# Optimization experiments

Hardware: AMD Instinct MI355X
Metric: run time of the kernel (lower is better)

Reference implementation:

```python
import jax, jax.numpy as jnp
import numpy as np

N = 50000      # nodes (atoms)
E = 800000     # edges (avg degree 16)
Z = 10         # num_elements
C = 32         # hidden channels (scalar multiplicity of hidden_irreps)
NB = 8         # num_bessel
H = 64         # radial MLP hidden
CORR = 3       # correlation order of product basis
MLPH = 16      # MLP_irreps = 16x0e
R_MAX = 5.0
AVG_NN = 16.0
P_CUT = 5      # num_polynomial_cutoff
N_SH = 9       # spherical harmonics up to l=2
L_OF_LM = jnp.array([0, 1, 1, 1, 2, 2, 2, 2, 2])  # l index of each lm component


def _sph_harm(u):
    # real spherical harmonics, e3nn 'component' normalization, up to l=2. u: [E,3] unit vectors
    x, y, z = u[:, 0], u[:, 1], u[:, 2]
    s3, s5, s15 = 3.0 ** 0.5, 5.0 ** 0.5, 15.0 ** 0.5
    return jnp.stack([
        jnp.ones_like(x),
        s3 * x, s3 * y, s3 * z,
        s15 * x * y, s15 * y * z, 0.5 * s5 * (3.0 * z * z - 1.0),
        s15 * x * z, 0.5 * s15 * (x * x - y * y),
    ], axis=-1)


def _poly_cutoff(r):
    # polynomial envelope, p=5, zero beyond r_max
    p = float(P_CUT)
    u = r / R_MAX
    f = (1.0 - 0.5 * (p + 1.0) * (p + 2.0) * u ** P_CUT
         + p * (p + 2.0) * u ** (P_CUT + 1)
         - 0.5 * p * (p + 1.0) * u ** (P_CUT + 2))
    return f * (u < 1.0)


def setup_inputs() -> dict:
    key = jax.random.key(0)
    ks = jax.random.split(key, 24)
    elems = jax.random.randint(ks[0], (N,), 0, Z)
    node_attrs = jax.nn.one_hot(elems, Z, dtype=jnp.float32)
    positions = jax.random.uniform(ks[1], (N, 3), dtype=jnp.float32, minval=0.0, maxval=10.0)
    senders = jax.random.randint(ks[2], (E,), 0, N)
    receivers = jax.random.randint(ks[3], (E,), 0, N)

    def rn(k, shape, fan_in):
        return jax.random.normal(k, shape, dtype=jnp.float32) / np.sqrt(fan_in)

    params = {
        'W_embed': rn(ks[4], (Z, C), Z),
        'atomic_E': jax.random.normal(ks[5], (Z,), dtype=jnp.float32),
        'Wr0': rn(ks[6], (2, NB, H), NB),
        'Wr1': rn(ks[7], (2, H, H), H),
        'Wr2': rn(ks[8], (2, H, H), H),
        'Wr3': rn(ks[9], (2, H, 3 * C), H),
        'Wlin': rn(ks[10], (2, C, C), C),
        'Wsc': rn(ks[11], (2, Z, C, C), C),
        'Wprod': rn(ks[12], (2, 3, C, C), C),
        'Wp': rn(ks[13], (2, CORR, Z, C), Z),
        'w_ro1': rn(ks[14], (C,), C),
        'W_m1': rn(ks[15], (C, MLPH), C),
        'w_m2': rn(ks[16], (MLPH,), MLPH),
    }
    return {'node_attrs': node_attrs, 'positions': positions,
            'senders': senders, 'receivers': receivers, **params}


def reference(node_attrs, positions, W_embed, atomic_E, Wr0, Wr1, Wr2, Wr3,
              Wlin, Wsc, Wprod, Wp, w_ro1, W_m1, w_m2, senders, receivers):
    silu = jax.nn.silu
    # --- edge geometry ---
    vec = positions[receivers] - positions[senders]          # [E,3]
    r = jnp.sqrt(jnp.sum(vec * vec, axis=-1) + 1e-12)        # [E]
    unit = vec / r[:, None]
    sh = _sph_harm(unit)                                     # [E, 9]
    fcut = _poly_cutoff(r)                                   # [E]

    # --- radial embedding: Bessel basis * polynomial cutoff ---
    n = jnp.arange(1, NB + 1, dtype=jnp.float32)
    bessel = jnp.sqrt(2.0 / R_MAX) * jnp.sin(n[None, :] * jnp.pi * r[:, None] / R_MAX) / r[:, None]
    R = bessel * fcut[:, None]                               # [E, NB]

    # --- ZBL pair repulsion ---
    z_arr = jnp.arange(1, Z + 1, dtype=jnp.float32)
    zq = node_attrs @ z_arr                                  # [N]
    zi, zj = zq[senders], zq[receivers]
    a = 0.46850 / (zi ** 0.23 + zj ** 0.23)
    xx = r / a
    phi = (0.1818 * jnp.exp(-3.2 * xx) + 0.5099 * jnp.exp(-0.9423 * xx)
           + 0.2802 * jnp.exp(-0.4029 * xx) + 0.02817 * jnp.exp(-0.2016 * xx))
    v_zbl = 14.3996 * zi * zj / r * phi * fcut
    pair_energy = 0.5 * jax.ops.segment_sum(v_zbl, receivers, num_segments=N)  # [N]

    # --- atomic reference energies + node embedding ---
    node_energy = node_attrs @ atomic_E + pair_energy        # [N]
    h = node_attrs @ W_embed                                 # [N, C] scalar node feats

    feats_list = []
    for i in range(2):
        # radial MLP -> per-edge, per-l, per-channel tensor-product weights
        w = silu(R @ Wr0[i])
        w = silu(w @ Wr1[i])
        w = silu(w @ Wr2[i])
        w = (w @ Wr3[i]).reshape(E, 3, C)                    # [E, l, C]
        w_lm = w[:, L_OF_LM, :]                              # [E, 9, C]
        # message: channel-mixed sender scalars x spherical harmonics x radial weights
        h1 = h @ Wlin[i]                                     # [N, C]
        msg = sh[:, :, None] * h1[senders][:, None, :] * w_lm  # [E, 9, C]
        A = jax.ops.segment_sum(msg, receivers, num_segments=N) / AVG_NN  # [N, 9, C]
        # element-conditioned residual (self-connection)
        sc = jnp.einsum('nz,nc,zcd->nd', node_attrs, h, Wsc[i])  # [N, C]
        # equivariant product basis: per-l linear + symmetric contraction on scalars
        Wlm = Wprod[i][L_OF_LM]                              # [9, C, C]
        out = jnp.einsum('nmc,mcd->nmd', A, Wlm)             # [N, 9, C]
        A0 = A[:, 0, :]
        poly = jnp.zeros_like(A0)
        for k in range(CORR):
            poly = poly + jnp.einsum('nz,zc->nc', node_attrs, Wp[i, k]) * A0 ** (k + 1)
        h_scalar = out[:, 0, :] + poly + sc                  # [N, C]
        # readout
        if i == 0:
            e = h_scalar @ w_ro1
        else:
            e = silu(h_scalar @ W_m1) @ w_m2
        node_energy = node_energy + e
        h = h_scalar
        feats_list.append(out.at[:, 0, :].set(h_scalar).reshape(N, N_SH * C))

    node_feats = jnp.concatenate(feats_list, axis=-1)        # [N, 2*9*C]
    return node_energy, node_feats
```

## Files before the change

### kernel.cpp

```cpp
#include <hip/hip_runtime.h>
#include <math.h>

static constexpr int Cdim = 32;
static constexpr int NBES = 8;
static constexpr int HDIM = 64;
static constexpr int ZDIM = 10;
static constexpr int TBLN = 8192;

typedef _Float16 half8 __attribute__((ext_vector_type(8)));
typedef _Float16 half4 __attribute__((ext_vector_type(4)));
typedef float floatx4 __attribute__((ext_vector_type(4)));

__device__ __forceinline__ float silu_f(float x) {
    return x / (1.0f + __expf(-x));
}

__device__ __forceinline__ float4 shfl4(float4 v, int src) {
    return make_float4(__shfl(v.x, src), __shfl(v.y, src),
                       __shfl(v.z, src), __shfl(v.w, src));
}

__global__ __launch_bounds__(320)
void k_wemb(const float* __restrict__ W_embed, const float* __restrict__ Wlin0,
            float* __restrict__ EW)
{
    int t = threadIdx.x;
    if (t >= ZDIM * Cdim) return;
    int z = t >> 5, d = t & 31;
    float acc = 0.f;
    #pragma unroll
    for (int c = 0; c < Cdim; ++c) acc += W_embed[z * Cdim + c] * Wlin0[c * Cdim + d];
    EW[t] = acc;
}

__global__ __launch_bounds__(256)
void k_node_init(const float* __restrict__ attrs, const float* __restrict__ pos,
                 const float* __restrict__ W_embed, const float* __restrict__ atomE,
                 const float* __restrict__ EW, int* __restrict__ elem,
                 float* __restrict__ energy, int* __restrict__ deg,
                 float4* __restrict__ pos4, _Float16* __restrict__ h16cur,
                 _Float16* __restrict__ h1a16, int N)
{
    int n = blockIdx.x * blockDim.x + threadIdx.x;
    if (n >= N) return;
    int e = 0; float best = -1.0f;
    #pragma unroll
    for (int z = 0; z < ZDIM; ++z) {
        float v = attrs[n * ZDIM + z];
        if (v > best) { best = v; e = z; }
    }
    elem[n] = e;
    #pragma unroll
    for (int c = 0; c < Cdim; c += 4) {
        half4 ph, p1;
        #pragma unroll
        for (int q = 0; q < 4; ++q) {
            ph[q] = (_Float16)W_embed[e * Cdim + c + q];
            p1[q] = (_Float16)EW[e * Cdim + c + q];
        }
        *(half4*)(h16cur + (size_t)n * Cdim + c) = ph;
        *(half4*)(h1a16  + (size_t)n * Cdim + c) = p1;
    }
    energy[n] = atomE[e];
    deg[n] = 0;
    float zf = (float)(e + 1);
    pos4[n] = make_float4(pos[3*n+0], pos[3*n+1], pos[3*n+2],
                          4.0f * zf + powf(zf, 0.23f));
}

__global__ __launch_bounds__(256)
void k_filter(const float4* __restrict__ pos4, const int* __restrict__ snd,
              const int* __restrict__ rcv, unsigned long long* __restrict__ mask,
              int* __restrict__ deg, float4* __restrict__ quadE,
              float* __restrict__ zslotE, int E)
{
    int e = blockIdx.x * blockDim.x + threadIdx.x;
    int ec = min(e, E - 1);
    int s = snd[ec], t = rcv[ec];
    float4 pt = pos4[t], ps = pos4[s];
    float dx = pt.x - ps.x, dy = pt.y - ps.y, dz = pt.z - ps.z;
    float d2 = dx*dx + dy*dy + dz*dz;
    bool pred = (e < E) && (d2 < 25.0f);
    unsigned long long m = __ballot(pred ? 1 : 0);
    if ((threadIdx.x & 63) == 0) mask[e >> 6] = m;
    if (pred) {
        atomicAdd(&deg[t], 1);
        float r  = sqrtf(d2 + 1e-12f);
        float inv_r = 1.0f / r;
        quadE[e] = make_float4(dx * inv_r, dy * inv_r, dz * inv_r, r);
        float tz = floorf(pt.w * 0.25f), tz23 = pt.w - 4.0f * tz;
        float sz = floorf(ps.w * 0.25f), sz23 = ps.w - 4.0f * sz;
        float u  = r * 0.2f;
        float u2 = u*u, u5 = u2*u2*u;
        float fcut = 1.0f - 21.0f*u5 + 35.0f*u5*u - 15.0f*u5*u2;
        float xx = r * (sz23 + tz23) * 2.134471718f;
        float phi = 0.1818f*__expf(-3.2f*xx) + 0.5099f*__expf(-0.9423f*xx)
                  + 0.2802f*__expf(-0.4029f*xx) + 0.02817f*__expf(-0.2016f*xx);
        zslotE[e] = tz * sz * inv_r * phi * fcut;
    }
}

__global__ __launch_bounds__(1024)
void k_scan1(const int* __restrict__ deg, int* __restrict__ rowptr,
             int* __restrict__ bsum, int* __restrict__ bhist,
             int* __restrict__ myslot, int N)
{
    __shared__ int wsum[16];
    __shared__ int lhist[64];
    int tid = threadIdx.x, lane = tid & 63, w = tid >> 6;
    if (tid < 64) lhist[tid] = 0;
    __syncthreads();
    int i = blockIdx.x * 1024 + tid;
    int v = (i < N) ? deg[i] : 0;
    if (i < N) myslot[i] = atomicAdd(&lhist[min(v, 63)], 1);
    int s = v;
    #pragma unroll
    for (int d = 1; d < 64; d <<= 1) {
        int u = __shfl_up(s, d);
        if (lane >= d) s += u;
    }
    if (lane == 63) wsum[w] = s;
    __syncthreads();
    if (w == 0 && lane < 16) {
        int x = wsum[lane];
        #pragma unroll
        for (int d = 1; d < 16; d <<= 1) {
            int u = __shfl_up(x, d);
            if (lane >= d) x += u;
        }
        wsum[lane] = x;
    }
    __syncthreads();
    int wave_off = (w == 0) ? 0 : wsum[w - 1];
    if (i < N) rowptr[i] = wave_off + (s - v);
    if (tid == 0) bsum[blockIdx.x] = wsum[15];
    if (tid < 64) bhist[blockIdx.x * 64 + tid] = lhist[tid];
}

__global__ __launch_bounds__(128)
void k_scan2(int* __restrict__ bsum, int nb, int* __restrict__ bhist,
             int* __restrict__ rowptrN)
{
    int tid = threadIdx.x;
    int lane = tid & 63;
    if (tid < 64) {
        int v = (lane < nb) ? bsum[lane] : 0;
        int s = v;
        #pragma unroll
        for (int d = 1; d < 64; d <<= 1) {
            int u = __shfl_up(s, d);
            if (lane >= d) s += u;
        }
        if (lane < nb) bsum[lane] = s - v;
        if (lane == 63) *rowptrN = s;
    } else {
        int b = lane;
        int run = 0;
        for (int blk = 0; blk < nb; ++blk) {
            int t = bhist[blk * 64 + b];
            bhist[blk * 64 + b] = run;
            run += t;
        }
        int s = run;
        #pragma unroll
        for (int d = 1; d < 64; d <<= 1) {
            int u = __shfl_up(s, d);
            if (lane >= d) s += u;
        }
        int excl = s - run;
        for (int blk = 0; blk < nb; ++blk) bhist[blk * 64 + b] += excl;
    }
}

__global__ __launch_bounds__(1024)
void k_scan3(const int* __restrict__ deg, int* __restrict__ rowptr,
             int* __restrict__ cursor, const int* __restrict__ bsum,
             const int* __restrict__ bhist, const int* __restrict__ myslot,
             int* __restrict__ perm, int N)
{
    int i = blockIdx.x * 1024 + threadIdx.x;
    if (i >= N) return;
    int rv = rowptr[i] + bsum[blockIdx.x];
    rowptr[i] = rv;
    cursor[i] = rv;
    int b = min(deg[i], 63);
    perm[bhist[blockIdx.x * 64 + b] + myslot[i]] = i;
}

__global__ __launch_bounds__(256)
void k_place(const int* __restrict__ snd, const int* __restrict__ rcv,
             const unsigned long long* __restrict__ mask,
             const float4* __restrict__ quadE, const float* __restrict__ zslotE,
             int* __restrict__ cursor, int* __restrict__ eS,
             float4* __restrict__ quad, float* __restrict__ zslot, int E)
{
    int e = blockIdx.x * blockDim.x + threadIdx.x;
    if (e >= E) return;
    if (!((mask[e >> 6] >> (e & 63)) & 1ull)) return;
    int t = rcv[e];
    int slot = atomicAdd(&cursor[t], 1);
    eS[slot] = snd[e];
    quad[slot] = quadE[e];
    zslot[slot] = zslotE[e];
}

__global__ __launch_bounds__(256, 2)
void k_table(const float* __restrict__ W0, const float* __restrict__ W1,
             const float* __restrict__ W2, const float* __restrict__ W3,
             _Float16* __restrict__ table)
{
    __shared__ __align__(16) _Float16 sWt0[64*32];
    __shared__ __align__(16) _Float16 sWt1[64*64];
    __shared__ __align__(16) _Float16 sWt2[64*64];
    __shared__ __align__(16) _Float16 sWt3[96*64];
    __shared__ __align__(16) _Float16 sAct[4][64*64];

    for (int idx = threadIdx.x; idx < 64*32; idx += 256) {
        int n = idx >> 5, k = idx & 31;
        float v = (k < NBES) ? W0[k*64 + n] : 0.f;
        *(_Float16*)((char*)sWt0 + n*64 + ((k*2) ^ ((n&3)<<4))) = (_Float16)v;
    }
    for (int idx = threadIdx.x; idx < 64*64; idx += 256) {
        int k = idx >> 6, n = idx & 63;
        int byo = n*128 + ((k*2) ^ ((n&7)<<4));
        *(_Float16*)((char*)sWt1 + byo) = (_Float16)W1[idx];
        *(_Float16*)((char*)sWt2 + byo) = (_Float16)W2[idx];
    }
    for (int idx = threadIdx.x; idx < 64*96; idx += 256) {
        int k = idx / 96, n = idx - k*96;
        *(_Float16*)((char*)sWt3 + n*128 + ((k*2) ^ ((n&7)<<4))) = (_Float16)W3[idx];
    }
    __syncthreads();

    const int wid = threadIdx.x >> 6, lane = threadIdx.x & 63;
    const int l15 = lane & 15, lh = lane >> 4;
    char* actc = (char*)sAct[wid];

    half8 w1f[4], w2f[4][2], w3f[4][2], w4f[6][2];
    #pragma unroll
    for (int nt = 0; nt < 4; ++nt) {
        int nn = nt*16 + l15;
        w1f[nt] = *(half8*)((char*)sWt0 + nn*64 + ((lh*16) ^ ((nn&3)<<4)));
        #pragma unroll
        for (int ks = 0; ks < 2; ++ks) {
            w2f[nt][ks] = *(half8*)((char*)sWt1 + nn*128 + ((ks*64 + lh*16) ^ ((nn&7)<<4)));
            w3f[nt][ks] = *(half8*)((char*)sWt2 + nn*128 + ((ks*64 + lh*16) ^ ((nn&7)<<4)));
        }
    }
    #pragma unroll
    for (int nt = 0; nt < 6; ++nt) {
        int nn = nt*16 + l15;
        #pragma unroll
        for (int ks = 0; ks < 2; ++ks)
            w4f[nt][ks] = *(half8*)((char*)sWt3 + nn*128 + ((ks*64 + lh*16) ^ ((nn&7)<<4)));
    }

    int c0 = (blockIdx.x*4 + wid)*64;
    {
        int q = c0 + lane;
        float r = (q + 0.5f) * (5.0f / (float)TBLN);
        float inv_r = 1.0f / r;
        float u  = r * 0.2f;
        float u2 = u*u, u5 = u2*u2*u;
        float fcut = 1.0f - 21.0f*u5 + 35.0f*u5*u - 15.0f*u5*u2;
        float coef = 0.632455532f * inv_r * fcut;
        half8 rv;
        #pragma unroll
        for (int j = 0; j < NBES; ++j)
            rv[j] = (_Float16)(coef * __sinf((float)(j+1) * 0.628318531f * r));
        {
            int sw = (lane & 7) << 4;
            half8 zz = {};
            *(half8*)(actc + lane*128 + ( 0 ^ sw)) = rv;
            *(half8*)(actc + lane*128 + (16 ^ sw)) = zz;
            *(half8*)(actc + lane*128 + (32 ^ sw)) = zz;
            *(half8*)(actc + lane*128 + (48 ^ sw)) = zz;
        }
        __builtin_amdgcn_sched_barrier(0);

        #pragma unroll
        for (int mt = 0; mt < 4; ++mt) {
            int rr = mt*16 + l15;
            int swz = (rr & 7) << 4;
            half8 act = *(half8*)(actc + rr*128 + ((lh*16) ^ swz));
            #pragma unroll
            for (int nt = 0; nt < 4; ++nt) {
                floatx4 z = {0.f,0.f,0.f,0.f};
                floatx4 d = __builtin_amdgcn_mfma_f32_16x16x32_f16(w1f[nt], act, z, 0,0,0);
                half4 pk;
                #pragma unroll
                for (int j = 0; j < 4; ++j) pk[j] = (_Float16)silu_f(d[j]);
                *(half4*)(actc + rr*128 + ((nt*32 + lh*8) ^ swz)) = pk;
            }
        }
        __builtin_amdgcn_sched_barrier(0);

        #pragma unroll
        for (int layer = 0; layer < 2; ++layer) {
            #pragma unroll
            for (int mt = 0; mt < 4; ++mt) {
                int rr = mt*16 + l15;
                int swz = (rr & 7) << 4;
                half8 a0 = *(half8*)(actc + rr*128 + ((      lh*16) ^ swz));
                half8 a1 = *(half8*)(actc + rr*128 + ((64 + lh*16) ^ swz));
                #pragma unroll
                for (int nt = 0; nt < 4; ++nt) {
                    floatx4 z = {0.f,0.f,0.f,0.f};
                    if (layer == 0) {
                        z = __builtin_amdgcn_mfma_f32_16x16x32_f16(w2f[nt][0], a0, z, 0,0,0);
                        z = __builtin_amdgcn_mfma_f32_16x16x32_f16(w2f[nt][1], a1, z, 0,0,0);
                    } else {
                        z = __builtin_amdgcn_mfma_f32_16x16x32_f16(w3f[nt][0], a0, z, 0,0,0);
                        z = __builtin_amdgcn_mfma_f32_16x16x32_f16(w3f[nt][1], a1, z, 0,0,0);
                    }
                    half4 pk;
                    #pragma unroll
                    for (int j = 0; j < 4; ++j) pk[j] = (_Float16)silu_f(z[j]);
                    *(half4*)(actc + rr*128 + ((nt*32 + lh*8) ^ swz)) = pk;
                }
            }
            __builtin_amdgcn_sched_barrier(0);
        }

        #pragma unroll
        for (int mt = 0; mt < 4; ++mt) {
            int rr = mt*16 + l15;
            int swz = (rr & 7) << 4;
            half8 a0 = *(half8*)(actc + rr*128 + ((      lh*16) ^ swz));
            half8 a1 = *(half8*)(actc + rr*128 + ((64 + lh*16) ^ swz));
            int e = c0 + rr;
            #pragma unroll
            for (int nt = 0; nt < 6; ++nt) {
                floatx4 z = {0.f,0.f,0.f,0.f};
                z = __builtin_amdgcn_mfma_f32_16x16x32_f16(w4f[nt][0], a0, z, 0,0,0);
                z = __builtin_amdgcn_mfma_f32_16x16x32_f16(w4f[nt][1], a1, z, 0,0,0);
                half4 pk;
                #pragma unroll
                for (int j = 0; j < 4; ++j) pk[j] = (_Float16)z[j];
                *(half4*)(table + (size_t)e*96 + nt*16 + lh*4) = pk;
            }
        }
    }
}

template<int ITER>
__global__ __launch_bounds__(256, 4)
void k_gather_epi(const int* __restrict__ rowptr, const int* __restrict__ eS,
                  const float4* __restrict__ quad, const float* __restrict__ zslot,
                  const _Float16* __restrict__ h1_16, const _Float16* __restrict__ hcur16,
                  const _Float16* __restrict__ table, const int* __restrict__ perm,
                  float* AO, const int* __restrict__ elem,
                  const float* __restrict__ Wprod, const float* __restrict__ Wsc,
                  const float* __restrict__ Wp, const float* __restrict__ w_ro1,
                  const float* __restrict__ W_m1, const float* __restrict__ w_m2,
                  const float* __restrict__ Wlin_next, _Float16* __restrict__ h1_next16,
                  _Float16* __restrict__ hcur_next16,
                  float* __restrict__ energy, int N)
{
    __shared__ float sWp[1024];
    __shared__ __align__(16) _Float16 sWt16[2048];
    __shared__ float sM1[(ITER == 1) ? 512 : 16];
    __shared__ float sm2[16];
    __shared__ float sro[32];
    __shared__ float sWl[(ITER == 0) ? 1024 : 16];
    __shared__ __align__(16) _Float16 sA16[32 * 296];
    __shared__ int sPerm[32];

    for (int t = threadIdx.x; t < 1024; t += 256) sWp[t] = Wprod[t];
    for (int t = threadIdx.x; t < 2048; t += 256) {
        int l = t >> 10, rem = t & 1023, d = rem >> 5, c = rem & 31;
        *(_Float16*)((char*)sWt16 + l*2048 + d*64 + ((c*2) ^ ((d&3)<<4))) =
            (_Float16)Wprod[(l + 1) * 1024 + c * 32 + d];
    }
    if (ITER == 1)
        for (int t = threadIdx.x; t < 512; t += 256) sM1[t] = W_m1[t];
    if (ITER == 0)
        for (int t = threadIdx.x; t < 1024; t += 256) sWl[t] = Wlin_next[t];
    if (threadIdx.x < 16) sm2[threadIdx.x] = w_m2[threadIdx.x];
    if (threadIdx.x < 32) {
        sro[threadIdx.x] = w_ro1[threadIdx.x];
        int idx = blockIdx.x * 32 + threadIdx.x;
        sPerm[threadIdx.x] = (idx < N) ? perm[idx] : -1;
    }
    __syncthreads();

    int lane = threadIdx.x & 63;
    int gbase = lane & 56;
    int g = threadIdx.x >> 3, j = threadIdx.x & 7, c0 = j * 4;
    int n = sPerm[g];
    bool valid = (n >= 0);

    float acc[9][4];
    #pragma unroll
    for (int m = 0; m < 9; ++m)
        #pragma unroll
        for (int q = 0; q < 4; ++q) acc[m][q] = 0.f;
    float zacc = 0.f;

    if (valid) {
        int lo = rowptr[n], hi = rowptr[n+1];

        for (int base = lo; base < hi; base += 2) {
            int k0 = base;
            bool v1 = (base + 1 < hi);
            int k1 = v1 ? (base + 1) : k0;

            float4 qd0 = quad[k0];
            float4 qd1 = quad[k1];
            int s0 = eS[k0];
            int s1 = eS[k1];

            int i00 = min((int)(qd0.w * ((float)TBLN / 5.0f)), TBLN - 1);
            int i10 = min((int)(qd1.w * ((float)TBLN / 5.0f)), TBLN - 1);

            const _Float16* T00 = table + (size_t)i00 * 96 + c0;
            const _Float16* T10 = table + (size_t)i10 * 96 + c0;
            half4 e0a0 = *(const half4*)(T00);
            half4 e0a1 = *(const half4*)(T00 + 32);
            half4 e0a2 = *(const half4*)(T00 + 64);
            half4 e1a0 = *(const half4*)(T10);
            half4 e1a1 = *(const half4*)(T10 + 32);
            half4 e1a2 = *(const half4*)(T10 + 64);

            half4 hv0 = *(const half4*)(h1_16 + (size_t)s0 * Cdim + c0);
            half4 hv1 = *(const half4*)(h1_16 + (size_t)s1 * Cdim + c0);

            float vf1 = v1 ? 1.0f : 0.0f;

            if (ITER == 0) {
                zacc += zslot[k0];
                zacc += vf1 * zslot[k1];
            }

            {
                float ux = qd0.x, uy = qd0.y, uz = qd0.z;
                const float s3 = 1.73205081f, s5 = 2.23606798f, s15 = 3.87298335f;
                float sh1 = s3 * ux, sh2 = s3 * uy, sh3 = s3 * uz;
                float sh4 = s15 * ux * uy, sh5 = s15 * uy * uz;
                float sh6 = 0.5f * s5 * (3.0f * uz * uz - 1.0f);
                float sh7 = s15 * ux * uz;
                float sh8 = 0.5f * s15 * (ux * ux - uy * uy);

                #pragma unroll
                for (int q = 0; q < 4; ++q) {
                    float hb = (float)hv0[q];
                    float m0 = hb * (float)e0a0[q];
                    float m1 = hb * (float)e0a1[q];
                    float m2 = hb * (float)e0a2[q];
                    acc[0][q] += m0;
                    acc[1][q] += sh1 * m1;
                    acc[2][q] += sh2 * m1;
                    acc[3][q] += sh3 * m1;
                    acc[4][q] += sh4 * m2;
                    acc[5][q] += sh5 * m2;
                    acc[6][q] += sh6 * m2;
                    acc[7][q] += sh7 * m2;
                    acc[8][q] += sh8 * m2;
                }
            }
            {
                float ux = qd1.x, uy = qd1.y, uz = qd1.z;
                const float s3 = 1.73205081f, s5 = 2.23606798f, s15 = 3.87298335f;
                float sh1 = s3 * ux, sh2 = s3 * uy, sh3 = s3 * uz;
                float sh4 = s15 * ux * uy, sh5 = s15 * uy * uz;
                float sh6 = 0.5f * s5 * (3.0f * uz * uz - 1.0f);
                float sh7 = s15 * ux * uz;
                float sh8 = 0.5f * s15 * (ux * ux - uy * uy);

                #pragma unroll
                for (int q = 0; q < 4; ++q) {
                    float hb = (float)hv1[q] * vf1;
                    float m0 = hb * (float)e1a0[q];
                    float m1 = hb * (float)e1a1[q];
                    float m2 = hb * (float)e1a2[q];
                    acc[0][q] += m0;
                    acc[1][q] += sh1 * m1;
                    acc[2][q] += sh2 * m1;
                    acc[3][q] += sh3 * m1;
                    acc[4][q] += sh4 * m2;
                    acc[5][q] += sh5 * m2;
                    acc[6][q] += sh6 * m2;
                    acc[7][q] += sh7 * m2;
                    acc[8][q] += sh8 * m2;
                }
            }
        }

        #pragma unroll
        for (int m = 1; m <= 8; ++m) {
            half4 pk;
            #pragma unroll
            for (int q = 0; q < 4; ++q) pk[q] = (_Float16)(acc[m][q] * 0.0625f);
            *(half4*)((char*)sA16 + g * 592 + m * 64 + j * 8) = pk;
        }
    }
    __syncthreads();

    {
        int w = threadIdx.x >> 6;
        int l15 = lane & 15, lh = lane >> 4;
        int nhalf = (w >> 1) * 16;
        int mbase = (w & 1) * 4 + 1;
        int node = sPerm[nhalf + l15];
        const int outslot = (ITER == 0) ? 0 : 288;

        half8 af[2][2];
        #pragma unroll
        for (int l = 0; l < 2; ++l)
            #pragma unroll
            for (int nt = 0; nt < 2; ++nt) {
                int row = nt * 16 + l15;
                af[l][nt] = *(half8*)((char*)sWt16 + l*2048 + row*64 +
                                      ((lh*16) ^ ((row&3)<<4)));
            }
        #pragma unroll
        for (int mi = 0; mi < 4; ++mi) {
            int m = mbase + mi;
            int l = (m <= 3) ? 0 : 1;
            half8 bf = *(half8*)((char*)sA16 + (nhalf + l15) * 592 + m * 64 + lh * 16);
            #pragma unroll
            for (int nt = 0; nt < 2; ++nt) {
                floatx4 z = {0.f, 0.f, 0.f, 0.f};
                z = __builtin_amdgcn_mfma_f32_16x16x32_f16(af[l][nt], bf, z, 0, 0, 0);
                if (node >= 0)
                    *(floatx4*)(AO + (size_t)node * 576 + outslot + m * 32 +
                                nt * 16 + lh * 4) = z;
            }
        }
    }

    if (valid) {
        int el = elem[n];
        half4 hq4 = *(const half4*)(hcur16 + (size_t)n * Cdim + c0);
        float4 hown = make_float4((float)hq4[0], (float)hq4[1],
                                  (float)hq4[2], (float)hq4[3]);
        float4 A0own = make_float4(acc[0][0]*0.0625f, acc[0][1]*0.0625f,
                                   acc[0][2]*0.0625f, acc[0][3]*0.0625f);
        const float* Ws = Wsc + (size_t)el * 1024;
        float hs[4] = {0.f, 0.f, 0.f, 0.f};

        #pragma unroll
        for (int j2 = 0; j2 < 8; ++j2) {
            int src = gbase + j2;
            float4 a4 = shfl4(A0own, src);
            float4 h4 = shfl4(hown, src);
            float aq[4] = {a4.x, a4.y, a4.z, a4.w};
            float hq[4] = {h4.x, h4.y, h4.z, h4.w};
            #pragma unroll
            for (int q = 0; q < 4; ++q) {
                int c = j2 * 4 + q;
                float4 wp = *(const float4*)&sWp[c * 32 + c0];
                float4 wv = *(const float4*)(Ws + c * 32 + c0);
                hs[0] += aq[q] * wp.x + hq[q] * wv.x;
                hs[1] += aq[q] * wp.y + hq[q] * wv.y;
                hs[2] += aq[q] * wp.z + hq[q] * wv.z;
                hs[3] += aq[q] * wp.w + hq[q] * wv.w;
            }
        }
        {
            const float* wpb = Wp + el * 32;
            float4 p1 = *(const float4*)(wpb + c0);
            float4 p2 = *(const float4*)(wpb + 320 + c0);
            float4 p3 = *(const float4*)(wpb + 640 + c0);
            float p1a[4] = {p1.x, p1.y, p1.z, p1.w};
            float p2a[4] = {p2.x, p2.y, p2.z, p2.w};
            float p3a[4] = {p3.x, p3.y, p3.z, p3.w};
            #pragma unroll
            for (int d = 0; d < 4; ++d) {
                float A = acc[0][d] * 0.0625f, A2 = A * A;
                hs[d] += p1a[d] * A + p2a[d] * A2 + p3a[d] * (A2 * A);
            }
        }

        float eadd;
        if (ITER == 0) {
            float a = hs[0]*sro[c0] + hs[1]*sro[c0+1] + hs[2]*sro[c0+2] + hs[3]*sro[c0+3];
            a += __shfl_xor(a, 1); a += __shfl_xor(a, 2); a += __shfl_xor(a, 4);
            eadd = a + 7.1998f * zacc;
        } else {
            float tj[16];
            #pragma unroll
            for (int q = 0; q < 16; ++q) {
                float tv = 0.f;
                #pragma unroll
                for (int d = 0; d < 4; ++d) tv += hs[d] * sM1[(c0 + d) * 16 + q];
                tv += __shfl_xor(tv, 1); tv += __shfl_xor(tv, 2); tv += __shfl_xor(tv, 4);
                tj[q] = tv;
            }
            float a = 0.f;
            #pragma unroll
            for (int q = 0; q < 16; ++q) a += silu_f(tj[q]) * sm2[q];
            eadd = a;
        }
        if (j == 0) energy[n] += eadd;

        const int outslot = (ITER == 0) ? 0 : 288;
        *(float4*)(AO + (size_t)n * 576 + outslot + c0) = make_float4(hs[0], hs[1], hs[2], hs[3]);

        if (ITER == 0) {
            half4 ph;
            #pragma unroll
            for (int q = 0; q < 4; ++q) ph[q] = (_Float16)hs[q];
            *(half4*)(hcur_next16 + (size_t)n * Cdim + c0) = ph;

            float4 hsv = make_float4(hs[0], hs[1], hs[2], hs[3]);
            float o[4] = {0.f, 0.f, 0.f, 0.f};
            #pragma unroll
            for (int j2 = 0; j2 < 8; ++j2) {
                float4 h4 = shfl4(hsv, gbase + j2);
                float hq[4] = {h4.x, h4.y, h4.z, h4.w};
                #pragma unroll
                for (int q = 0; q < 4; ++q) {
                    float4 wv = *(const float4*)&sWl[(j2 * 4 + q) * 32 + c0];
                    o[0] += hq[q] * wv.x; o[1] += hq[q] * wv.y;
                    o[2] += hq[q] * wv.z; o[3] += hq[q] * wv.w;
                }
            }
            half4 p1;
            #pragma unroll
            for (int q = 0; q < 4; ++q) p1[q] = (_Float16)o[q];
            *(half4*)(h1_next16 + (size_t)n * Cdim + c0) = p1;
        }
    }
}

extern "C" void kernel_launch(void* const* d_in, const int* in_sizes, int n_in,
                              void* d_out, int out_size, void* d_ws, size_t ws_size,
                              hipStream_t stream)
{
    const float* attrs   = (const float*)d_in[0];
    const float* pos     = (const float*)d_in[1];
    const int*   snd     = (const int*)d_in[2];
    const int*   rcv     = (const int*)d_in[3];
    const float* W_embed = (const float*)d_in[4];
    const float* atomE   = (const float*)d_in[5];
    const float* Wr0     = (const float*)d_in[6];
    const float* Wr1     = (const float*)d_in[7];
    const float* Wr2     = (const float*)d_in[8];
    const float* Wr3     = (const float*)d_in[9];
    const float* Wlin    = (const float*)d_in[10];
    const float* Wsc     = (const float*)d_in[11];
    const float* Wprod   = (const float*)d_in[12];
    const float* Wp      = (const float*)d_in[13];
    const float* w_ro1   = (const float*)d_in[14];
    const float* W_m1    = (const float*)d_in[15];
    const float* w_m2    = (const float*)d_in[16];

    const int N = in_sizes[1] / 3;
    const int E = in_sizes[2];

    float* energy = (float*)d_out;
    float* feats  = (float*)d_out + N;

    char* ws = (char*)d_ws;
    size_t off = 0;
    auto alloc = [&](size_t bytes) { void* p = ws + off; off = (off + bytes + 255) & ~(size_t)255; return p; };
    int*  deg    = (int*)alloc((size_t)N * 4);
    int*  cursor = (int*)alloc((size_t)N * 4);
    int*  rowptr = (int*)alloc((size_t)(N + 1) * 4);
    unsigned long long* mask = (unsigned long long*)alloc((size_t)((E + 63) / 64) * 8);
    int*  eS     = (int*)alloc((size_t)E * 4);
    float4* quad = (float4*)alloc((size_t)E * 16);
    float* zslot = (float*)alloc((size_t)E * 4);
    float4* quadE = (float4*)alloc((size_t)E * 16);
    float* zslotE = (float*)alloc((size_t)E * 4);
    int*  elem   = (int*)alloc((size_t)N * 4);
    float4* pos4 = (float4*)alloc((size_t)N * 16);
    _Float16* h16cur = (_Float16*)alloc((size_t)N * Cdim * 2);
    _Float16* h16b   = (_Float16*)alloc((size_t)N * Cdim * 2);
    _Float16* h1a16  = (_Float16*)alloc((size_t)N * Cdim * 2);
    _Float16* h1b16  = (_Float16*)alloc((size_t)N * Cdim * 2);
    float* EW    = (float*)alloc((size_t)ZDIM * Cdim * 4);
    _Float16* table = (_Float16*)alloc((size_t)TBLN * 96 * 2);
    int* bsum   = (int*)alloc(64 * 4);
    int* bhist  = (int*)alloc(64 * 64 * 4);
    int* myslot = (int*)alloc((size_t)N * 4);
    int* perm   = (int*)alloc((size_t)N * 4);

    const int NB1024 = (N + 1023) / 1024;

    k_wemb<<<1, 320, 0, stream>>>(W_embed, Wlin, EW);
    k_node_init<<<(N + 255)/256, 256, 0, stream>>>(attrs, pos, W_embed, atomE, EW, elem,
                                                   energy, deg, pos4, h16cur, h1a16, N);
    k_filter<<<(E + 255)/256, 256, 0, stream>>>(pos4, snd, rcv, mask, deg, quadE, zslotE, E);
    k_scan1<<<NB1024, 1024, 0, stream>>>(deg, rowptr, bsum, bhist, myslot, N);
    k_scan2<<<1, 128, 0, stream>>>(bsum, NB1024, bhist, rowptr + N);
    k_scan3<<<NB1024, 1024, 0, stream>>>(deg, rowptr, cursor, bsum, bhist, myslot, perm, N);
    k_place<<<(E + 255)/256, 256, 0, stream>>>(snd, rcv, mask, quadE, zslotE,
                                               cursor, eS, quad, zslot, E);

    const int NBLK = (N + 31) / 32;

    k_table<<<TBLN/256, 256, 0, stream>>>(Wr0, Wr1, Wr2, Wr3, table);
    k_gather_epi<0><<<NBLK, 256, 0, stream>>>(rowptr, eS, quad, zslot, h1a16, h16cur, table,
        perm, feats, elem, Wprod, Wsc, Wp, w_ro1, W_m1, w_m2,
        Wlin + 1024, h1b16, h16b, energy, N);

    k_table<<<TBLN/256, 256, 0, stream>>>(Wr0 + NBES * HDIM, Wr1 + HDIM * HDIM,
        Wr2 + HDIM * HDIM, Wr3 + HDIM * 96, table);
    k_gather_epi<1><<<NBLK, 256, 0, stream>>>(rowptr, eS, quad, zslot, h1b16, h16b, table,
        perm, feats, elem, Wprod + 3072, Wsc + 10240, Wp + 960, w_ro1, W_m1, w_m2,
        Wlin, h1b16, h16b, energy, N);
}
```

Before: 202.7 us.

## Split each node's edge gather across two thread groups and fuse embedding-weight precompute

The gather kernel now gives 16 threads to each node instead of 8. Two halves take interleaved pairs of edges and combine their accumulators with a cross-lane xor shuffle, so a block covers 16 nodes and twice as many blocks launch. The MFMA product stage is re-split so each of the four waves handles two lm components for the 16 nodes, and the launch-bounds occupancy hint goes from 4 to 6. The separate k_wemb launch is folded into k_node_init, where every block recomputes the small embedding×Wlin product into shared memory. This is meant to shorten per-thread serial edge loops and raise occupancy, at the cost of extra shuffles, idle half-groups in the epilogue, and redundant per-block weight work.

New measurement: 374.6 us. 1.85x slower.

```diff
diff --git a/kernel.cpp b/kernel.cpp
--- a/kernel.cpp
+++ b/kernel.cpp
@@ -20,27 +20,23 @@
                        __shfl(v.z, src), __shfl(v.w, src));
 }
 
-__global__ __launch_bounds__(320)
-void k_wemb(const float* __restrict__ W_embed, const float* __restrict__ Wlin0,
-            float* __restrict__ EW)
-{
-    int t = threadIdx.x;
-    if (t >= ZDIM * Cdim) return;
-    int z = t >> 5, d = t & 31;
-    float acc = 0.f;
-    #pragma unroll
-    for (int c = 0; c < Cdim; ++c) acc += W_embed[z * Cdim + c] * Wlin0[c * Cdim + d];
-    EW[t] = acc;
-}
-
 __global__ __launch_bounds__(256)
 void k_node_init(const float* __restrict__ attrs, const float* __restrict__ pos,
                  const float* __restrict__ W_embed, const float* __restrict__ atomE,
-                 const float* __restrict__ EW, int* __restrict__ elem,
+                 const float* __restrict__ Wlin0, int* __restrict__ elem,
                  float* __restrict__ energy, int* __restrict__ deg,
                  float4* __restrict__ pos4, _Float16* __restrict__ h16cur,
                  _Float16* __restrict__ h1a16, int N)
 {
+    __shared__ float sEW[ZDIM * Cdim];
+    for (int t = threadIdx.x; t < ZDIM * Cdim; t += 256) {
+        int z = t >> 5, d = t & 31;
+        float acc = 0.f;
+        #pragma unroll
+        for (int c = 0; c < Cdim; ++c) acc += W_embed[z * Cdim + c] * Wlin0[c * Cdim + d];
+        sEW[t] = acc;
+    }
+    __syncthreads();
     int n = blockIdx.x * blockDim.x + threadIdx.x;
     if (n >= N) return;
     int e = 0; float best = -1.0f;
@@ -56,7 +52,7 @@
         #pragma unroll
         for (int q = 0; q < 4; ++q) {
             ph[q] = (_Float16)W_embed[e * Cdim + c + q];
-            p1[q] = (_Float16)EW[e * Cdim + c + q];
+            p1[q] = (_Float16)sEW[e * Cdim + c + q];
         }
         *(half4*)(h16cur + (size_t)n * Cdim + c) = ph;
         *(half4*)(h1a16  + (size_t)n * Cdim + c) = p1;
@@ -344,7 +340,7 @@
 }
 
 template<int ITER>
-__global__ __launch_bounds__(256, 4)
+__global__ __launch_bounds__(256, 6)
 void k_gather_epi(const int* __restrict__ rowptr, const int* __restrict__ eS,
                   const float4* __restrict__ quad, const float* __restrict__ zslot,
                   const _Float16* __restrict__ h1_16, const _Float16* __restrict__ hcur16,
@@ -363,8 +359,8 @@
     __shared__ float sm2[16];
     __shared__ float sro[32];
     __shared__ float sWl[(ITER == 0) ? 1024 : 16];
-    __shared__ __align__(16) _Float16 sA16[32 * 296];
-    __shared__ int sPerm[32];
+    __shared__ __align__(16) _Float16 sA16[16 * 296];
+    __shared__ int sPerm[16];
 
     for (int t = threadIdx.x; t < 1024; t += 256) sWp[t] = Wprod[t];
     for (int t = threadIdx.x; t < 2048; t += 256) {
@@ -376,18 +372,21 @@
         for (int t = threadIdx.x; t < 512; t += 256) sM1[t] = W_m1[t];
     if (ITER == 0)
         for (int t = threadIdx.x; t < 1024; t += 256) sWl[t] = Wlin_next[t];
-    if (threadIdx.x < 16) sm2[threadIdx.x] = w_m2[threadIdx.x];
-    if (threadIdx.x < 32) {
-        sro[threadIdx.x] = w_ro1[threadIdx.x];
-        int idx = blockIdx.x * 32 + threadIdx.x;
+    if (threadIdx.x < 16) {
+        sm2[threadIdx.x] = w_m2[threadIdx.x];
+        int idx = blockIdx.x * 16 + threadIdx.x;
         sPerm[threadIdx.x] = (idx < N) ? perm[idx] : -1;
     }
+    if (threadIdx.x < 32) sro[threadIdx.x] = w_ro1[threadIdx.x];
     __syncthreads();
 
     int lane = threadIdx.x & 63;
-    int gbase = lane & 56;
-    int g = threadIdx.x >> 3, j = threadIdx.x & 7, c0 = j * 4;
-    int n = sPerm[g];
+    int gb = lane & 48;
+    int g16 = threadIdx.x >> 4;
+    int jj = threadIdx.x & 15;
+    int j = jj & 7, c0 = j * 4;
+    int half = jj >> 3;
+    int n = sPerm[g16];
     bool valid = (n >= 0);
 
     float acc[9][4];
@@ -400,7 +399,7 @@
     if (valid) {
         int lo = rowptr[n], hi = rowptr[n+1];
 
-        for (int base = lo; base < hi; base += 2) {
+        for (int base = lo + half * 2; base < hi; base += 4) {
             int k0 = base;
             bool v1 = (base + 1 < hi);
             int k1 = v1 ? (base + 1) : k0;
@@ -487,11 +486,20 @@
         }
 
         #pragma unroll
-        for (int m = 1; m <= 8; ++m) {
-            half4 pk;
-            #pragma unroll
-            for (int q = 0; q < 4; ++q) pk[q] = (_Float16)(acc[m][q] * 0.0625f);
-            *(half4*)((char*)sA16 + g * 592 + m * 64 + j * 8) = pk;
+        for (int m = 0; m < 9; ++m)
+            #pragma unroll
+            for (int q = 0; q < 4; ++q)
+                acc[m][q] += __shfl_xor(acc[m][q], 8);
+        if (ITER == 0) zacc += __shfl_xor(zacc, 8);
+
+        if (half == 0) {
+            #pragma unroll
+            for (int m = 1; m <= 8; ++m) {
+                half4 pk;
+                #pragma unroll
+                for (int q = 0; q < 4; ++q) pk[q] = (_Float16)(acc[m][q] * 0.0625f);
+                *(half4*)((char*)sA16 + g16 * 592 + m * 64 + j * 8) = pk;
+            }
         }
     }
     __syncthreads();
@@ -499,9 +507,7 @@
     {
         int w = threadIdx.x >> 6;
         int l15 = lane & 15, lh = lane >> 4;
-        int nhalf = (w >> 1) * 16;
-        int mbase = (w & 1) * 4 + 1;
-        int node = sPerm[nhalf + l15];
+        int node = sPerm[l15];
         const int outslot = (ITER == 0) ? 0 : 288;
 
         half8 af[2][2];
@@ -514,10 +520,10 @@
                                       ((lh*16) ^ ((row&3)<<4)));
             }
         #pragma unroll
-        for (int mi = 0; mi < 4; ++mi) {
-            int m = mbase + mi;
+        for (int mi = 0; mi < 2; ++mi) {
+            int m = w * 2 + 1 + mi;
             int l = (m <= 3) ? 0 : 1;
-            half8 bf = *(half8*)((char*)sA16 + (nhalf + l15) * 592 + m * 64 + lh * 16);
+            half8 bf = *(half8*)((char*)sA16 + l15 * 592 + m * 64 + lh * 16);
             #pragma unroll
             for (int nt = 0; nt < 2; ++nt) {
                 floatx4 z = {0.f, 0.f, 0.f, 0.f};
@@ -529,7 +535,7 @@
         }
     }
 
-    if (valid) {
+    if (valid && half == 0) {
         int el = elem[n];
         half4 hq4 = *(const half4*)(hcur16 + (size_t)n * Cdim + c0);
         float4 hown = make_float4((float)hq4[0], (float)hq4[1],
@@ -541,7 +547,7 @@
 
         #pragma unroll
         for (int j2 = 0; j2 < 8; ++j2) {
-            int src = gbase + j2;
+            int src = gb + j2;
             float4 a4 = shfl4(A0own, src);
             float4 h4 = shfl4(hown, src);
             float aq[4] = {a4.x, a4.y, a4.z, a4.w};
@@ -607,7 +613,7 @@
             float o[4] = {0.f, 0.f, 0.f, 0.f};
             #pragma unroll
             for (int j2 = 0; j2 < 8; ++j2) {
-                float4 h4 = shfl4(hsv, gbase + j2);
+                float4 h4 = shfl4(hsv, gb + j2);
                 float hq[4] = {h4.x, h4.y, h4.z, h4.w};
                 #pragma unroll
                 for (int q = 0; q < 4; ++q) {
@@ -670,7 +676,6 @@
     _Float16* h16b   = (_Float16*)alloc((size_t)N * Cdim * 2);
     _Float16* h1a16  = (_Float16*)alloc((size_t)N * Cdim * 2);
     _Float16* h1b16  = (_Float16*)alloc((size_t)N * Cdim * 2);
-    float* EW    = (float*)alloc((size_t)ZDIM * Cdim * 4);
     _Float16* table = (_Float16*)alloc((size_t)TBLN * 96 * 2);
     int* bsum   = (int*)alloc(64 * 4);
     int* bhist  = (int*)alloc(64 * 64 * 4);
@@ -679,8 +684,7 @@
 
     const int NB1024 = (N + 1023) / 1024;
 
-    k_wemb<<<1, 320, 0, stream>>>(W_embed, Wlin, EW);
-    k_node_init<<<(N + 255)/256, 256, 0, stream>>>(attrs, pos, W_embed, atomE, EW, elem,
+    k_node_init<<<(N + 255)/256, 256, 0, stream>>>(attrs, pos, W_embed, atomE, Wlin, elem,
                                                    energy, deg, pos4, h16cur, h1a16, N);
     k_filter<<<(E + 255)/256, 256, 0, stream>>>(pos4, snd, rcv, mask, deg, quadE, zslotE, E);
     k_scan1<<<NB1024, 1024, 0, stream>>>(deg, rowptr, bsum, bhist, myslot, N);
@@ -689,7 +693,7 @@
     k_place<<<(E + 255)/256, 256, 0, stream>>>(snd, rcv, mask, quadE, zslotE,
                                                cursor, eS, quad, zslot, E);
 
-    const int NBLK = (N + 31) / 32;
+    const int NBLK = (N + 15) / 16;
 
     k_table<<<TBLN/256, 256, 0, stream>>>(Wr0, Wr1, Wr2, Wr3, table);
     k_gather_epi<0><<<NBLK, 256, 0, stream>>>(rowptr, eS, quad, zslot, h1a16, h16cur, table,
```
